# Performance work log

Measured on AMD Instinct MI355X. Metric: run time of the kernel, lower is better.

The kernel has to match this reference:

```python
import jax, jax.numpy as jnp
import numpy as np

B, S, DM, H = 8, 1024, 1024, 16
D = DM // H  # head dim = 64


def setup_inputs() -> dict:
    key = jax.random.key(0)
    ks = jax.random.split(key, 10)
    Q = jax.random.normal(ks[0], (B, S, DM), jnp.float32)
    K = jax.random.normal(ks[1], (B, S, DM), jnp.float32)
    V = jax.random.normal(ks[2], (B, S, DM), jnp.float32)
    pad = jax.random.randint(ks[3], (B,), 0, 512)
    sc = 0.02
    Wq = jax.random.normal(ks[4], (H, DM, D), jnp.float32) * sc
    Wk = jax.random.normal(ks[5], (H, DM, D), jnp.float32) * sc
    Wv = jax.random.normal(ks[6], (H, DM, D), jnp.float32) * sc
    bq = jnp.zeros((H, D), jnp.float32)
    bk = jnp.zeros((H, D), jnp.float32)
    bv = jnp.zeros((H, D), jnp.float32)
    Wo = jax.random.normal(ks[7], (DM, DM), jnp.float32) * sc
    bo = jnp.zeros((DM,), jnp.float32)
    return {"Q": Q, "K": K, "V": V, "pad": pad,
            "Wq": Wq, "bq": bq, "Wk": Wk, "bk": bk,
            "Wv": Wv, "bv": bv, "Wo": Wo, "bo": bo}


def reference(Q, K, V, pad, Wq, bq, Wk, bk, Wv, bv, Wo, bo):
    seq = Q.shape[1]
    # per-head projections, batched over heads: [B,H,S,D]
    Qh = jnp.einsum('bsm,hmd->bhsd', Q, Wq) + bq[None, :, None, :]
    Kh = jnp.einsum('bsm,hmd->bhsd', K, Wk) + bk[None, :, None, :]
    Vh = jnp.einsum('bsm,hmd->bhsd', V, Wv) + bv[None, :, None, :]
    # NOTE: original divides by sqrt(seq_len) (K.shape[1]), not sqrt(head_dim)
    scores = jnp.einsum('bhsd,bhtd->bhst', Qh, Kh) / jnp.sqrt(jnp.float32(seq))
    t = jnp.arange(seq)
    # padding mask over keys: last pad[b] positions; pad==0 masks ALL (torch -0: quirk)
    pad_mask = (t[None, :] >= seq - pad[:, None]) | (pad[:, None] == 0)  # [B,T]
    causal = t[None, :] > t[:, None]  # [S,T], strict upper triangle
    M = jnp.maximum(pad_mask[:, None, None, :].astype(jnp.float32),
                    causal[None, None, :, :].astype(jnp.float32))
    scores = scores + M * (-1e9)
    att = jax.nn.softmax(scores, axis=-1)
    Xh = jnp.einsum('bhst,bhtd->bhsd', att, Vh)
    # concat heads along last dim (head order preserved)
    X = Xh.transpose(0, 2, 1, 3).reshape(Q.shape[0], seq, H * D)
    return X @ Wo + bo
```

## Files before the change

### kernel.cpp

```cpp
#include <hip/hip_runtime.h>
#include <cmath>

#define BATCH 8
#define SEQ 1024
#define DMODEL 1024
#define NHEAD 16
#define HDIM 64
#define USE_GLOAD 1

typedef _Float16 f16x8 __attribute__((ext_vector_type(8)));
typedef _Float16 f16x4 __attribute__((ext_vector_type(4)));
typedef _Float16 f16x2 __attribute__((ext_vector_type(2)));
typedef float    f32x4 __attribute__((ext_vector_type(4)));


__global__ __launch_bounds__(256)
void prep_cvt(const float* __restrict__ Q, const float* __restrict__ K,
              const float* __restrict__ V, _Float16* __restrict__ Qf,
              _Float16* __restrict__ Kf, _Float16* __restrict__ Vf)
{
    const int n = (8192 * 1024) / 4;
    const float*   src = (blockIdx.y == 0) ? Q : (blockIdx.y == 1) ? K : V;
    _Float16*      dst = (blockIdx.y == 0) ? Qf : (blockIdx.y == 1) ? Kf : Vf;
    for (int i = blockIdx.x * 256 + threadIdx.x; i < n; i += gridDim.x * 256) {
        const float4 v = ((const float4*)src)[i];
        ((f16x4*)dst)[i] = (f16x4){ (_Float16)v.x, (_Float16)v.y,
                                    (_Float16)v.z, (_Float16)v.w };
    }
}

__global__ __launch_bounds__(256)
void prep_tr(const float* __restrict__ Wq, const float* __restrict__ Wk,
             const float* __restrict__ Wv, const float* __restrict__ Wo,
             _Float16* __restrict__ WqT, _Float16* __restrict__ WkT,
             _Float16* __restrict__ WvT, _Float16* __restrict__ WoT)
{
    __shared__ float L[64][65];
    const int z  = blockIdx.z;
    const int t  = threadIdx.x;
    const float*    W  = (z == 0) ? Wq : (z == 1) ? Wk : (z == 2) ? Wv : Wo;
    _Float16*       WT = (z == 0) ? WqT : (z == 1) ? WkT : (z == 2) ? WvT : WoT;
    const int k0 = blockIdx.y * 64;
    const int n0 = blockIdx.x * 64;
    const int kr = t >> 2, c4 = (t & 3) * 16;
    const float* src = (z < 3)
        ? &W[((size_t)blockIdx.x * DMODEL + (k0 + kr)) * HDIM + c4]
        : &W[(size_t)(k0 + kr) * DMODEL + n0 + c4];
    #pragma unroll
    for (int j = 0; j < 4; ++j) {
        const float4 v = *(const float4*)(src + j * 4);
        L[kr][c4 + j * 4 + 0] = v.x; L[kr][c4 + j * 4 + 1] = v.y;
        L[kr][c4 + j * 4 + 2] = v.z; L[kr][c4 + j * 4 + 3] = v.w;
    }
    __syncthreads();
    const int d = t >> 2, kk = (t & 3) * 16;
    f16x8 o0, o1;
    #pragma unroll
    for (int j = 0; j < 8; ++j) {
        o0[j] = (_Float16)L[kk + j][d];
        o1[j] = (_Float16)L[kk + 8 + j][d];
    }
    *(f16x8*)&WT[(size_t)(n0 + d) * DMODEL + k0 + kk]     = o0;
    *(f16x8*)&WT[(size_t)(n0 + d) * DMODEL + k0 + kk + 8] = o1;
}

__global__ __launch_bounds__(256)
void transpose_v(const _Float16* __restrict__ Vh, _Float16* __restrict__ VT)
{
    __shared__ _Float16 L[64][72];
    const int bh = blockIdx.y;
    const int s0 = blockIdx.x * 64;
    const int t  = threadIdx.x;
    const size_t base = (size_t)bh * SEQ * HDIM;
    {
        const _Float16* src = &Vh[base + (size_t)(s0 + (t >> 2)) * HDIM + (t & 3) * 16];
        *(f16x8*)&L[t >> 2][(t & 3) * 16]     = *(const f16x8*)src;
        *(f16x8*)&L[t >> 2][(t & 3) * 16 + 8] = *(const f16x8*)(src + 8);
    }
    __syncthreads();
    const int d = t >> 2, sq = (t & 3) * 16;
    f16x8 o0, o1;
    #pragma unroll
    for (int j = 0; j < 8; ++j) {
        o0[j] = L[sq + j][d];
        o1[j] = L[sq + 8 + j][d];
    }
    _Float16* dst = &VT[base + (size_t)d * SEQ + s0 + sq];
    *(f16x8*)dst       = o0;
    *(f16x8*)(dst + 8) = o1;
}

template<int OLAYOUT>
__global__ __launch_bounds__(256)
void gemm_f16(const _Float16* __restrict__ A, const _Float16* __restrict__ BT,
              const float* __restrict__ bias, float* __restrict__ Cf,
              _Float16* __restrict__ Ch)
{
    constexpr int Kd = DMODEL;
    alignas(16) __shared__ _Float16 Al[128 * 64];
    alignas(16) __shared__ _Float16 Bl[128 * 64];

    const int t    = threadIdx.x;
    const int lane = t & 63;
    const int w    = t >> 6;
    const int wr   = w >> 1, wc = w & 1;
    const int q    = lane >> 4, r = lane & 15;
    const int m0   = blockIdx.y * 128;
    const int n0   = blockIdx.x * 128;
    const int srow = lane >> 3;
    const int sslot = lane & 7;

    f32x4 acc[4][4];
    #pragma unroll
    for (int i = 0; i < 4; ++i)
        #pragma unroll
        for (int j = 0; j < 4; ++j)
            acc[i][j] = (f32x4){0.f, 0.f, 0.f, 0.f};

    for (int kt = 0; kt < Kd / 64; ++kt) {
        const int k0 = kt * 64;
        #pragma unroll
        for (int j = 0; j < 4; ++j) {
            const int rowA = w * 32 + j * 8 + srow;
            const int colA = ((sslot ^ (rowA & 7)) << 3);
            __builtin_amdgcn_global_load_lds(
                (const __attribute__((address_space(1))) void*)
                    &A[(size_t)(m0 + rowA) * Kd + k0 + colA],
                (__attribute__((address_space(3))) void*)&Al[(w * 32 + j * 8) * 64],
                16, 0, 0);
        }
        #pragma unroll
        for (int j = 0; j < 4; ++j) {
            const int rowB = w * 32 + j * 8 + srow;
            const int colB = ((sslot ^ (rowB & 7)) << 3);
            __builtin_amdgcn_global_load_lds(
                (const __attribute__((address_space(1))) void*)
                    &BT[(size_t)(n0 + rowB) * Kd + k0 + colB],
                (__attribute__((address_space(3))) void*)&Bl[(w * 32 + j * 8) * 64],
                16, 0, 0);
        }
        __syncthreads();
        #pragma unroll
        for (int h = 0; h < 2; ++h) {
            f16x8 a[4], b[4];
            #pragma unroll
            for (int mf = 0; mf < 4; ++mf) {
                const int row = wr * 64 + mf * 16 + r;
                a[mf] = *(const f16x8*)&Al[row * 64 + (((h * 4 + q) ^ (row & 7)) << 3)];
            }
            #pragma unroll
            for (int nf = 0; nf < 4; ++nf) {
                const int row = wc * 64 + nf * 16 + r;
                b[nf] = *(const f16x8*)&Bl[row * 64 + (((h * 4 + q) ^ (row & 7)) << 3)];
            }
            #pragma unroll
            for (int mf = 0; mf < 4; ++mf)
                #pragma unroll
                for (int nf = 0; nf < 4; ++nf)
                    acc[mf][nf] = __builtin_amdgcn_mfma_f32_16x16x32_f16(
                        a[mf], b[nf], acc[mf][nf], 0, 0, 0);
        }
        __syncthreads();
    }

    #pragma unroll
    for (int mf = 0; mf < 4; ++mf) {
        #pragma unroll
        for (int nf = 0; nf < 4; ++nf) {
            const int col = n0 + wc * 64 + nf * 16 + r;
            const float bv = bias[col];
            #pragma unroll
            for (int i = 0; i < 4; ++i) {
                const int row = m0 + wr * 64 + mf * 16 + q * 4 + i;
                const float val = acc[mf][nf][i] + bv;
                if (OLAYOUT == 0) {
                    const int bb = row >> 10, s = row & 1023;
                    const int h = col >> 6, d = col & 63;
                    Ch[((((size_t)bb * NHEAD + h) << 10) + s) * HDIM + d] = (_Float16)val;
                } else {
                    Cf[(size_t)row * DMODEL + col] = val;
                }
            }
        }
    }
}

__global__ __launch_bounds__(256)
void attn_mfma(const _Float16* __restrict__ Qh, const _Float16* __restrict__ Kh,
               const _Float16* __restrict__ VT, const int* __restrict__ pad,
               _Float16* __restrict__ X)
{
    alignas(16) __shared__ _Float16 Klds[64 * 64];
    alignas(16) __shared__ _Float16 Vlds[64 * 64];
    alignas(16) __shared__ _Float16 Plds[4][16 * 64];

    const int tid  = threadIdx.x;
    const int w    = tid >> 6;
    const int lane = tid & 63;
    const int qq   = lane >> 4;
    const int r    = lane & 15;
    const int bh   = blockIdx.y;
    const int b    = bh >> 4;
    const int hh   = bh & 15;
    const int s0   = blockIdx.x << 6;
    const int padb = pad[b];
    const size_t base = (size_t)bh * SEQ * HDIM;
    const int mrow = s0 + w * 16;

    f16x8 qf[2];
    #pragma unroll
    for (int kh = 0; kh < 2; ++kh)
        qf[kh] = *(const f16x8*)&Qh[base + (size_t)(mrow + r) * HDIM + kh * 32 + qq * 8];

    const int kvlim = (padb == 0) ? SEQ : (SEQ - padb);
    const int Lblk  = (padb == 0) ? SEQ : min(s0 + 64, SEQ - padb);
    const int nt    = (Lblk + 63) >> 6;

    float mrun[4], lrun[4];
    f32x4 accO[4];
    #pragma unroll
    for (int i = 0; i < 4; ++i) {
        mrun[i] = -3.0e38f; lrun[i] = 0.f;
        accO[i] = (f32x4){0.f, 0.f, 0.f, 0.f};
    }

    const int srow  = lane >> 3;
    const int sslot = lane & 7;

    for (int kt = 0; kt < nt; ++kt) {
        const int t0 = kt << 6;
        __syncthreads();
        #pragma unroll
        for (int j = 0; j < 2; ++j) {
            const int row = j * 32 + w * 8 + srow;
            const int col = ((sslot ^ (row & 7)) << 3);
            __builtin_amdgcn_global_load_lds(
                (const __attribute__((address_space(1))) void*)
                    &Kh[base + (size_t)(t0 + row) * HDIM + col],
                (__attribute__((address_space(3))) void*)&Klds[(j * 32 + w * 8) * 64],
                16, 0, 0);
        }
        #pragma unroll
        for (int j = 0; j < 2; ++j) {
            const int row = j * 32 + w * 8 + srow;
            const int col = ((sslot ^ (row & 7)) << 3);
            __builtin_amdgcn_global_load_lds(
                (const __attribute__((address_space(1))) void*)
                    &VT[base + (size_t)row * SEQ + t0 + col],
                (__attribute__((address_space(3))) void*)&Vlds[(j * 32 + w * 8) * 64],
                16, 0, 0);
        }
        __syncthreads();

        f32x4 sacc[4];
        #pragma unroll
        for (int tg = 0; tg < 4; ++tg) sacc[tg] = (f32x4){0.f, 0.f, 0.f, 0.f};
        #pragma unroll
        for (int tg = 0; tg < 4; ++tg)
            #pragma unroll
            for (int kh = 0; kh < 2; ++kh) {
                const int kr = tg * 16 + r;
                const f16x8 kf = *(const f16x8*)
                    &Klds[kr * 64 + (((kh * 4 + qq) ^ (kr & 7)) << 3)];
                sacc[tg] = __builtin_amdgcn_mfma_f32_16x16x32_f16(qf[kh], kf, sacc[tg], 0, 0, 0);
            }

        float sc[4][4];
        #pragma unroll
        for (int tg = 0; tg < 4; ++tg) {
            const int tt = t0 + tg * 16 + r;
            #pragma unroll
            for (int i = 0; i < 4; ++i) {
                const int mm = mrow + qq * 4 + i;
                float x = sacc[tg][i] * 0.03125f;
                if (tt > mm || tt >= kvlim || padb == 0)
                    x -= 1.0e9f;
                sc[tg][i] = x;
            }
        }
        float p[4][4], scale[4];
        #pragma unroll
        for (int i = 0; i < 4; ++i) {
            float mx = fmaxf(fmaxf(sc[0][i], sc[1][i]), fmaxf(sc[2][i], sc[3][i]));
            #pragma unroll
            for (int off = 1; off < 16; off <<= 1)
                mx = fmaxf(mx, __shfl_xor(mx, off));
            const float mn = fmaxf(mrun[i], mx);
            scale[i] = __expf(mrun[i] - mn);
            mrun[i] = mn;
            float ls = 0.f;
            #pragma unroll
            for (int tg = 0; tg < 4; ++tg) {
                const float pv = __expf(sc[tg][i] - mn);
                p[tg][i] = pv;
                ls += pv;
            }
            #pragma unroll
            for (int off = 1; off < 16; off <<= 1)
                ls += __shfl_xor(ls, off);
            lrun[i] = lrun[i] * scale[i] + ls;
        }

        #pragma unroll
        for (int tg = 0; tg < 4; ++tg)
            #pragma unroll
            for (int i = 0; i < 4; ++i) {
                const int m  = qq * 4 + i;
                const int tt = tg * 16 + r;
                Plds[w][m * 64 + (((tt >> 3) ^ (m & 7)) << 3) + (tt & 7)] =
                    (_Float16)p[tg][i];
            }
        asm volatile("s_waitcnt lgkmcnt(0)" ::: "memory");
        __builtin_amdgcn_wave_barrier();

        f16x8 pa[2];
        #pragma unroll
        for (int kh = 0; kh < 2; ++kh)
            pa[kh] = *(const f16x8*)
                &Plds[w][r * 64 + (((kh * 4 + qq) ^ (r & 7)) << 3)];

        #pragma unroll
        for (int dg = 0; dg < 4; ++dg) {
            #pragma unroll
            for (int i = 0; i < 4; ++i) accO[dg][i] *= scale[i];
            #pragma unroll
            for (int kh = 0; kh < 2; ++kh) {
                const int vrow = dg * 16 + r;
                const f16x8 vf = *(const f16x8*)
                    &Vlds[vrow * 64 + (((kh * 4 + qq) ^ (vrow & 7)) << 3)];
                accO[dg] = __builtin_amdgcn_mfma_f32_16x16x32_f16(pa[kh], vf, accO[dg], 0, 0, 0);
            }
        }
    }

    #pragma unroll
    for (int dg = 0; dg < 4; ++dg)
        #pragma unroll
        for (int i = 0; i < 4; ++i)
            X[((size_t)b * SEQ + (mrow + qq * 4 + i)) * DMODEL + hh * HDIM + dg * 16 + r] =
                (_Float16)(accO[dg][i] / lrun[i]);
}

extern "C" void kernel_launch(void* const* d_in, const int* in_sizes, int n_in,
                              void* d_out, int out_size, void* d_ws, size_t ws_size,
                              hipStream_t stream)
{
    const float* Q  = (const float*)d_in[0];
    const float* K  = (const float*)d_in[1];
    const float* V  = (const float*)d_in[2];
    const int*  pad = (const int*)d_in[3];
    const float* Wq = (const float*)d_in[4];
    const float* bq = (const float*)d_in[5];
    const float* Wk = (const float*)d_in[6];
    const float* bk = (const float*)d_in[7];
    const float* Wv = (const float*)d_in[8];
    const float* bv = (const float*)d_in[9];
    const float* Wo = (const float*)d_in[10];
    const float* bo = (const float*)d_in[11];
    float* out = (float*)d_out;

    char* ws = (char*)d_ws;
    const size_t MB = 1024 * 1024;
    _Float16* Qf16 = (_Float16*)(ws + 0 * MB);
    _Float16* Kf16 = (_Float16*)(ws + 16 * MB);
    _Float16* Vf16 = (_Float16*)(ws + 32 * MB);
    _Float16* WqT  = (_Float16*)(ws + 48 * MB);
    _Float16* WkT  = (_Float16*)(ws + 50 * MB);
    _Float16* WvT  = (_Float16*)(ws + 52 * MB);
    _Float16* WoT  = (_Float16*)(ws + 54 * MB);
    _Float16* Qh   = (_Float16*)(ws + 56 * MB);
    _Float16* Kh   = (_Float16*)(ws + 72 * MB);
    _Float16* Vh   = (_Float16*)(ws + 0 * MB);
    _Float16* VT   = (_Float16*)(ws + 16 * MB);
    _Float16* X    = (_Float16*)(ws + 32 * MB);

    prep_cvt<<<dim3(1024, 3), 256, 0, stream>>>(Q, K, V, Qf16, Kf16, Vf16);
    prep_tr <<<dim3(16, 16, 4), 256, 0, stream>>>(Wq, Wk, Wv, Wo, WqT, WkT, WvT, WoT);

    dim3 gg(DMODEL / 128, (BATCH * SEQ) / 128);
    gemm_f16<0><<<gg, 256, 0, stream>>>(Qf16, WqT, bq, nullptr, Qh);
    gemm_f16<0><<<gg, 256, 0, stream>>>(Kf16, WkT, bk, nullptr, Kh);
    gemm_f16<0><<<gg, 256, 0, stream>>>(Vf16, WvT, bv, nullptr, Vh);

    transpose_v<<<dim3(SEQ / 64, BATCH * NHEAD), 256, 0, stream>>>(Vh, VT);

    attn_mfma<<<dim3(SEQ / 64, BATCH * NHEAD), 256, 0, stream>>>(Qh, Kh, VT, pad, X);

    gemm_f16<1><<<gg, 256, 0, stream>>>(X, WoT, bo, out, nullptr);
}
```

Baseline: 371.4 us.

## Batch QKV projections into one launch and pair causal query tiles per block

```diff
diff --git a/kernel.cpp b/kernel.cpp
--- a/kernel.cpp
+++ b/kernel.cpp
@@ -6,7 +6,6 @@
 #define DMODEL 1024
 #define NHEAD 16
 #define HDIM 64
-#define USE_GLOAD 1
 
 typedef _Float16 f16x8 __attribute__((ext_vector_type(8)));
 typedef _Float16 f16x4 __attribute__((ext_vector_type(4)));
@@ -91,10 +90,10 @@
 }
 
 template<int OLAYOUT>
-__global__ __launch_bounds__(256)
-void gemm_f16(const _Float16* __restrict__ A, const _Float16* __restrict__ BT,
-              const float* __restrict__ bias, float* __restrict__ Cf,
-              _Float16* __restrict__ Ch)
+__device__ __forceinline__
+void gemm_body(const _Float16* __restrict__ A, const _Float16* __restrict__ BT,
+               const float* __restrict__ bias, float* __restrict__ Cf,
+               _Float16* __restrict__ Ch)
 {
     constexpr int Kd = DMODEL;
     alignas(16) __shared__ _Float16 Al[128 * 64];
@@ -186,6 +185,31 @@
 }
 
 __global__ __launch_bounds__(256)
+void gemm_qkv(const _Float16* __restrict__ Qf, const _Float16* __restrict__ Kf,
+              const _Float16* __restrict__ Vf,
+              const _Float16* __restrict__ WqT, const _Float16* __restrict__ WkT,
+              const _Float16* __restrict__ WvT,
+              const float* __restrict__ bq, const float* __restrict__ bk,
+              const float* __restrict__ bv,
+              _Float16* __restrict__ Qh, _Float16* __restrict__ Kh,
+              _Float16* __restrict__ Vh)
+{
+    const int z = blockIdx.z;
+    const _Float16* A  = (z == 0) ? Qf  : (z == 1) ? Kf  : Vf;
+    const _Float16* BT = (z == 0) ? WqT : (z == 1) ? WkT : WvT;
+    const float*  bias = (z == 0) ? bq  : (z == 1) ? bk  : bv;
+    _Float16*     Ch   = (z == 0) ? Qh  : (z == 1) ? Kh  : Vh;
+    gemm_body<0>(A, BT, bias, nullptr, Ch);
+}
+
+__global__ __launch_bounds__(256)
+void gemm_out(const _Float16* __restrict__ A, const _Float16* __restrict__ BT,
+              const float* __restrict__ bias, float* __restrict__ C)
+{
+    gemm_body<1>(A, BT, bias, C, nullptr);
+}
+
+__global__ __launch_bounds__(256)
 void attn_mfma(const _Float16* __restrict__ Qh, const _Float16* __restrict__ Kh,
                const _Float16* __restrict__ VT, const int* __restrict__ pad,
                _Float16* __restrict__ X)
@@ -199,146 +223,152 @@
     const int lane = tid & 63;
     const int qq   = lane >> 4;
     const int r    = lane & 15;
+    const int bx   = blockIdx.x;
     const int bh   = blockIdx.y;
     const int b    = bh >> 4;
     const int hh   = bh & 15;
-    const int s0   = blockIdx.x << 6;
     const int padb = pad[b];
     const size_t base = (size_t)bh * SEQ * HDIM;
-    const int mrow = s0 + w * 16;
-
-    f16x8 qf[2];
-    #pragma unroll
-    for (int kh = 0; kh < 2; ++kh)
-        qf[kh] = *(const f16x8*)&Qh[base + (size_t)(mrow + r) * HDIM + kh * 32 + qq * 8];
-
     const int kvlim = (padb == 0) ? SEQ : (SEQ - padb);
-    const int Lblk  = (padb == 0) ? SEQ : min(s0 + 64, SEQ - padb);
-    const int nt    = (Lblk + 63) >> 6;
-
-    float mrun[4], lrun[4];
-    f32x4 accO[4];
-    #pragma unroll
-    for (int i = 0; i < 4; ++i) {
-        mrun[i] = -3.0e38f; lrun[i] = 0.f;
-        accO[i] = (f32x4){0.f, 0.f, 0.f, 0.f};
-    }
 
     const int srow  = lane >> 3;
     const int sslot = lane & 7;
 
-    for (int kt = 0; kt < nt; ++kt) {
-        const int t0 = kt << 6;
-        __syncthreads();
-        #pragma unroll
-        for (int j = 0; j < 2; ++j) {
-            const int row = j * 32 + w * 8 + srow;
-            const int col = ((sslot ^ (row & 7)) << 3);
-            __builtin_amdgcn_global_load_lds(
-                (const __attribute__((address_space(1))) void*)
-                    &Kh[base + (size_t)(t0 + row) * HDIM + col],
-                (__attribute__((address_space(3))) void*)&Klds[(j * 32 + w * 8) * 64],
-                16, 0, 0);
-        }
-        #pragma unroll
-        for (int j = 0; j < 2; ++j) {
-            const int row = j * 32 + w * 8 + srow;
-            const int col = ((sslot ^ (row & 7)) << 3);
-            __builtin_amdgcn_global_load_lds(
-                (const __attribute__((address_space(1))) void*)
-                    &VT[base + (size_t)row * SEQ + t0 + col],
-                (__attribute__((address_space(3))) void*)&Vlds[(j * 32 + w * 8) * 64],
-                16, 0, 0);
-        }
-        __syncthreads();
-
-        f32x4 sacc[4];
-        #pragma unroll
-        for (int tg = 0; tg < 4; ++tg) sacc[tg] = (f32x4){0.f, 0.f, 0.f, 0.f};
-        #pragma unroll
-        for (int tg = 0; tg < 4; ++tg)
-            #pragma unroll
-            for (int kh = 0; kh < 2; ++kh) {
-                const int kr = tg * 16 + r;
-                const f16x8 kf = *(const f16x8*)
-                    &Klds[kr * 64 + (((kh * 4 + qq) ^ (kr & 7)) << 3)];
-                sacc[tg] = __builtin_amdgcn_mfma_f32_16x16x32_f16(qf[kh], kf, sacc[tg], 0, 0, 0);
-            }
-
-        float sc[4][4];
-        #pragma unroll
-        for (int tg = 0; tg < 4; ++tg) {
-            const int tt = t0 + tg * 16 + r;
+    #pragma unroll
+    for (int ph = 0; ph < 2; ++ph) {
+        const int qx   = (ph == 0) ? bx : (15 - bx);
+        const int s0   = qx << 6;
+        const int mrow = s0 + w * 16;
+
+        f16x8 qf[2];
+        #pragma unroll
+        for (int kh = 0; kh < 2; ++kh)
+            qf[kh] = *(const f16x8*)&Qh[base + (size_t)(mrow + r) * HDIM + kh * 32 + qq * 8];
+
+        const int Lblk = (padb == 0) ? SEQ : min(s0 + 64, kvlim);
+        const int nt   = (Lblk + 63) >> 6;
+
+        float mrun[4], lrun[4];
+        f32x4 accO[4];
+        #pragma unroll
+        for (int i = 0; i < 4; ++i) {
+            mrun[i] = -3.0e38f; lrun[i] = 0.f;
+            accO[i] = (f32x4){0.f, 0.f, 0.f, 0.f};
+        }
+
+        for (int kt = 0; kt < nt; ++kt) {
+            const int t0 = kt << 6;
+            __syncthreads();
+            #pragma unroll
+            for (int j = 0; j < 2; ++j) {
+                const int row = j * 32 + w * 8 + srow;
+                const int col = ((sslot ^ (row & 7)) << 3);
+                __builtin_amdgcn_global_load_lds(
+                    (const __attribute__((address_space(1))) void*)
+                        &Kh[base + (size_t)(t0 + row) * HDIM + col],
+                    (__attribute__((address_space(3))) void*)&Klds[(j * 32 + w * 8) * 64],
+                    16, 0, 0);
+            }
+            #pragma unroll
+            for (int j = 0; j < 2; ++j) {
+                const int row = j * 32 + w * 8 + srow;
+                const int col = ((sslot ^ (row & 7)) << 3);
+                __builtin_amdgcn_global_load_lds(
+                    (const __attribute__((address_space(1))) void*)
+                        &VT[base + (size_t)row * SEQ + t0 + col],
+                    (__attribute__((address_space(3))) void*)&Vlds[(j * 32 + w * 8) * 64],
+                    16, 0, 0);
+            }
+            __syncthreads();
+
+            f32x4 sacc[4];
+            #pragma unroll
+            for (int tg = 0; tg < 4; ++tg) sacc[tg] = (f32x4){0.f, 0.f, 0.f, 0.f};
+            #pragma unroll
+            for (int tg = 0; tg < 4; ++tg)
+                #pragma unroll
+                for (int kh = 0; kh < 2; ++kh) {
+                    const int kr = tg * 16 + r;
+                    const f16x8 kf = *(const f16x8*)
+                        &Klds[kr * 64 + (((kh * 4 + qq) ^ (kr & 7)) << 3)];
+                    sacc[tg] = __builtin_amdgcn_mfma_f32_16x16x32_f16(qf[kh], kf, sacc[tg], 0, 0, 0);
+                }
+
+            float sc[4][4];
+            #pragma unroll
+            for (int tg = 0; tg < 4; ++tg) {
+                const int tt = t0 + tg * 16 + r;
+                #pragma unroll
+                for (int i = 0; i < 4; ++i) {
+                    const int mm = mrow + qq * 4 + i;
+                    float x = sacc[tg][i] * 0.03125f;
+                    if (tt > mm || tt >= kvlim || padb == 0)
+                        x -= 1.0e9f;
+                    sc[tg][i] = x;
+                }
+            }
+            float p[4][4], scale[4];
             #pragma unroll
             for (int i = 0; i < 4; ++i) {
-                const int mm = mrow + qq * 4 + i;
-                float x = sacc[tg][i] * 0.03125f;
-                if (tt > mm || tt >= kvlim || padb == 0)
-                    x -= 1.0e9f;
-                sc[tg][i] = x;
-            }
-        }
-        float p[4][4], scale[4];
-        #pragma unroll
-        for (int i = 0; i < 4; ++i) {
-            float mx = fmaxf(fmaxf(sc[0][i], sc[1][i]), fmaxf(sc[2][i], sc[3][i]));
-            #pragma unroll
-            for (int off = 1; off < 16; off <<= 1)
-                mx = fmaxf(mx, __shfl_xor(mx, off));
-            const float mn = fmaxf(mrun[i], mx);
-            scale[i] = __expf(mrun[i] - mn);
-            mrun[i] = mn;
-            float ls = 0.f;
-            #pragma unroll
-            for (int tg = 0; tg < 4; ++tg) {
-                const float pv = __expf(sc[tg][i] - mn);
-                p[tg][i] = pv;
-                ls += pv;
-            }
-            #pragma unroll
-            for (int off = 1; off < 16; off <<= 1)
-                ls += __shfl_xor(ls, off);
-            lrun[i] = lrun[i] * scale[i] + ls;
-        }
-
-        #pragma unroll
-        for (int tg = 0; tg < 4; ++tg)
-            #pragma unroll
-            for (int i = 0; i < 4; ++i) {
-                const int m  = qq * 4 + i;
-                const int tt = tg * 16 + r;
-                Plds[w][m * 64 + (((tt >> 3) ^ (m & 7)) << 3) + (tt & 7)] =
-                    (_Float16)p[tg][i];
-            }
-        asm volatile("s_waitcnt lgkmcnt(0)" ::: "memory");
-        __builtin_amdgcn_wave_barrier();
-
-        f16x8 pa[2];
-        #pragma unroll
-        for (int kh = 0; kh < 2; ++kh)
-            pa[kh] = *(const f16x8*)
-                &Plds[w][r * 64 + (((kh * 4 + qq) ^ (r & 7)) << 3)];
-
-        #pragma unroll
-        for (int dg = 0; dg < 4; ++dg) {
-            #pragma unroll
-            for (int i = 0; i < 4; ++i) accO[dg][i] *= scale[i];
-            #pragma unroll
-            for (int kh = 0; kh < 2; ++kh) {
-                const int vrow = dg * 16 + r;
-                const f16x8 vf = *(const f16x8*)
-                    &Vlds[vrow * 64 + (((kh * 4 + qq) ^ (vrow & 7)) << 3)];
-                accO[dg] = __builtin_amdgcn_mfma_f32_16x16x32_f16(pa[kh], vf, accO[dg], 0, 0, 0);
-            }
-        }
-    }
-
-    #pragma unroll
-    for (int dg = 0; dg < 4; ++dg)
-        #pragma unroll
-        for (int i = 0; i < 4; ++i)
-            X[((size_t)b * SEQ + (mrow + qq * 4 + i)) * DMODEL + hh * HDIM + dg * 16 + r] =
-                (_Float16)(accO[dg][i] / lrun[i]);
+                float mx = fmaxf(fmaxf(sc[0][i], sc[1][i]), fmaxf(sc[2][i], sc[3][i]));
+                #pragma unroll
+                for (int off = 1; off < 16; off <<= 1)
+                    mx = fmaxf(mx, __shfl_xor(mx, off));
+                const float mn = fmaxf(mrun[i], mx);
+                scale[i] = __expf(mrun[i] - mn);
+                mrun[i] = mn;
+                float ls = 0.f;
+                #pragma unroll
+                for (int tg = 0; tg < 4; ++tg) {
+                    const float pv = __expf(sc[tg][i] - mn);
+                    p[tg][i] = pv;
+                    ls += pv;
+                }
+                #pragma unroll
+                for (int off = 1; off < 16; off <<= 1)
+                    ls += __shfl_xor(ls, off);
+                lrun[i] = lrun[i] * scale[i] + ls;
+            }
+
+            #pragma unroll
+            for (int tg = 0; tg < 4; ++tg)
+                #pragma unroll
+                for (int i = 0; i < 4; ++i) {
+                    const int m  = qq * 4 + i;
+                    const int tt = tg * 16 + r;
+                    Plds[w][m * 64 + (((tt >> 3) ^ (m & 7)) << 3) + (tt & 7)] =
+                        (_Float16)p[tg][i];
+                }
+            asm volatile("s_waitcnt lgkmcnt(0)" ::: "memory");
+            __builtin_amdgcn_wave_barrier();
+
+            f16x8 pa[2];
+            #pragma unroll
+            for (int kh = 0; kh < 2; ++kh)
+                pa[kh] = *(const f16x8*)
+                    &Plds[w][r * 64 + (((kh * 4 + qq) ^ (r & 7)) << 3)];
+
+            #pragma unroll
+            for (int dg = 0; dg < 4; ++dg) {
+                #pragma unroll
+                for (int i = 0; i < 4; ++i) accO[dg][i] *= scale[i];
+                #pragma unroll
+                for (int kh = 0; kh < 2; ++kh) {
+                    const int vrow = dg * 16 + r;
+                    const f16x8 vf = *(const f16x8*)
+                        &Vlds[vrow * 64 + (((kh * 4 + qq) ^ (vrow & 7)) << 3)];
+                    accO[dg] = __builtin_amdgcn_mfma_f32_16x16x32_f16(pa[kh], vf, accO[dg], 0, 0, 0);
+                }
+            }
+        }
+
+        #pragma unroll
+        for (int dg = 0; dg < 4; ++dg)
+            #pragma unroll
+            for (int i = 0; i < 4; ++i)
+                X[((size_t)b * SEQ + (mrow + qq * 4 + i)) * DMODEL + hh * HDIM + dg * 16 + r] =
+                    (_Float16)(accO[dg][i] / lrun[i]);
+    }
 }
 
 extern "C" void kernel_launch(void* const* d_in, const int* in_sizes, int n_in,
@@ -377,14 +407,12 @@
     prep_cvt<<<dim3(1024, 3), 256, 0, stream>>>(Q, K, V, Qf16, Kf16, Vf16);
     prep_tr <<<dim3(16, 16, 4), 256, 0, stream>>>(Wq, Wk, Wv, Wo, WqT, WkT, WvT, WoT);
 
-    dim3 gg(DMODEL / 128, (BATCH * SEQ) / 128);
-    gemm_f16<0><<<gg, 256, 0, stream>>>(Qf16, WqT, bq, nullptr, Qh);
-    gemm_f16<0><<<gg, 256, 0, stream>>>(Kf16, WkT, bk, nullptr, Kh);
-    gemm_f16<0><<<gg, 256, 0, stream>>>(Vf16, WvT, bv, nullptr, Vh);
+    gemm_qkv<<<dim3(DMODEL / 128, (BATCH * SEQ) / 128, 3), 256, 0, stream>>>(
+        Qf16, Kf16, Vf16, WqT, WkT, WvT, bq, bk, bv, Qh, Kh, Vh);
 
     transpose_v<<<dim3(SEQ / 64, BATCH * NHEAD), 256, 0, stream>>>(Vh, VT);
 
-    attn_mfma<<<dim3(SEQ / 64, BATCH * NHEAD), 256, 0, stream>>>(Qh, Kh, VT, pad, X);
-
-    gemm_f16<1><<<gg, 256, 0, stream>>>(X, WoT, bo, out, nullptr);
-}
+    attn_mfma<<<dim3(8, BATCH * NHEAD), 256, 0, stream>>>(Qh, Kh, VT, pad, X);
+
+    gemm_out<<<dim3(DMODEL / 128, (BATCH * SEQ) / 128), 256, 0, stream>>>(X, WoT, bo, out);
+}
```

Result: faster. 356.2 us (-4.1%).
